# Performance work log

Measured on AMD Instinct MI355X. Metric: run time of the kernel, lower is better.

Reference implementation:

```python
import jax, jax.numpy as jnp
import numpy as np


def setup_inputs() -> dict:
    key = jax.random.key(0)
    k1, k2 = jax.random.split(key)
    decoder_output = jax.random.normal(k1, (8, 2048, 128), dtype=jnp.float32)
    encoder_output = jax.random.normal(k2, (8, 4096, 128), dtype=jnp.float32)
    return {"decoder_output": decoder_output, "encoder_output": encoder_output}


def reference(decoder_output, encoder_output):
    # Unscaled Luong (general dot) attention.
    # scores: [B, Tq, Tk] = dec [B,Tq,D] . enc [B,Tk,D]^T
    scores = jnp.einsum('bqd,bkd->bqk', decoder_output, encoder_output)
    attention = jax.nn.softmax(scores, axis=-1)
    # context: [B, Tq, D] = attn [B,Tq,Tk] . enc [B,Tk,D]
    context = jnp.einsum('bqk,bkd->bqd', attention, encoder_output)
    return (context, attention)
```

## Files before the change

kernel.cpp:

```cpp
#include <hip/hip_runtime.h>

using f16   = _Float16;
using f16x4 = __attribute__((ext_vector_type(4))) _Float16;
using f16x8 = __attribute__((ext_vector_type(8))) _Float16;
using f32x4 = __attribute__((ext_vector_type(4))) float;

#define NBATCH 8
#define TQ 2048
#define TK 4096
#define DD 128
#define QBLK 32
#define KBLK 128
#define NT (TK / KBLK)
#define CTX_ELEMS ((size_t)NBATCH * TQ * DD)
#define PWLD 56
#define CTLD 132

__device__ __forceinline__ int koff(int t, int d) {
    const int blk = ((t >> 2) & 3) ^ ((d >> 4) & 3);
    return (t >> 4) * 2304 + (d >> 4) * 288 + blk * 72 + (t & 3) * 16 + (d & 15);
}

__device__ __forceinline__ f16x4 ds_read_tr16(unsigned addr) {
    f16x4 d;
    asm volatile("ds_read_b64_tr_b16 %0, %1" : "=v"(d) : "v"(addr));
    return d;
}

__global__ __launch_bounds__(256)
void cvt_kernel(const float* __restrict__ in, f16* __restrict__ out) {
    const size_t i = ((size_t)blockIdx.x * 256 + threadIdx.x) * 8;
    const float4 a = *(const float4*)(in + i);
    const float4 b = *(const float4*)(in + i + 4);
    f16x8 h;
    h[0] = (f16)a.x; h[1] = (f16)a.y; h[2] = (f16)a.z; h[3] = (f16)a.w;
    h[4] = (f16)b.x; h[5] = (f16)b.y; h[6] = (f16)b.z; h[7] = (f16)b.w;
    *(f16x8*)(out + i) = h;
}

template<bool F16SRC>
__global__ __launch_bounds__(512, 4)
void luong_attn_kernel(const float* __restrict__ dec,
                       const void* __restrict__ encv,
                       float* __restrict__ out) {
    __shared__ __align__(16) char LDSbuf[36864 + 8 * 16 * PWLD * 2 + 512];
    f16*   Kt    = (f16*)LDSbuf;
    f16*   PwAll = (f16*)(LDSbuf + 36864);
    float* Zbuf  = (float*)(LDSbuf + 36864 + 8 * 16 * PWLD * 2);

    const int tid  = threadIdx.x;
    const int wid  = tid >> 6;
    const int lane = tid & 63;
    const int lo   = lane & 15;
    const int g    = lane >> 4;
    const int qg   = wid & 1;
    const int th   = wid >> 1;

    const int b     = blockIdx.x & 7;
    const int qbase = (blockIdx.x >> 3) * QBLK;

    const float* encB32 = F16SRC ? nullptr : ((const float*)encv) + (size_t)b * TK * DD;
    const f16*   encB16 = F16SRC ? ((const f16*)encv) + (size_t)b * TK * DD : nullptr;
    float* attn = out + CTX_ELEMS + ((size_t)b * TQ + qbase) * TK;

    auto stage = [&](int tile) {
        if constexpr (F16SRC) {
            const f16* src = encB16 + (size_t)tile * KBLK * DD;
            #pragma unroll
            for (int i = 0; i < 4; ++i) {
                const int c = tid + (i << 9);
                const int t = c >> 4;
                const int d0 = (c & 15) << 3;
                *(f16x8*)&Kt[koff(t, d0)] = *(const f16x8*)(src + t * DD + d0);
            }
        } else {
            const float* src = encB32 + (size_t)tile * KBLK * DD;
            #pragma unroll
            for (int i = 0; i < 8; ++i) {
                const int c = tid + (i << 9);
                const int t = c >> 5;
                const int d = (c & 31) << 2;
                const float4 v = *(const float4*)(src + t * DD + d);
                f16x4 h;
                h[0] = (f16)v.x; h[1] = (f16)v.y; h[2] = (f16)v.z; h[3] = (f16)v.w;
                *(f16x4*)&Kt[koff(t, d)] = h;
            }
        }
    };

    const float* qp = dec + ((size_t)b * TQ + qbase + qg * 16 + lo) * DD;
    f16x8 qf[4];
    #pragma unroll
    for (int kk = 0; kk < 4; ++kk) {
        const float4 x = *(const float4*)(qp + kk * 32 + g * 8);
        const float4 y = *(const float4*)(qp + kk * 32 + g * 8 + 4);
        f16x8 h;
        h[0] = (f16)x.x; h[1] = (f16)x.y; h[2] = (f16)x.z; h[3] = (f16)x.w;
        h[4] = (f16)y.x; h[5] = (f16)y.y; h[6] = (f16)y.z; h[7] = (f16)y.w;
        qf[kk] = h;
    }

    float Zp[4] = {0.f, 0.f, 0.f, 0.f};
    #pragma unroll 1
    for (int tile = 0; tile < NT; ++tile) {
        stage(tile);
        __syncthreads();

        f32x4 S[2];
        #pragma unroll
        for (int f = 0; f < 2; ++f) { f32x4 z = {0.f, 0.f, 0.f, 0.f}; S[f] = z; }
        #pragma unroll
        for (int f = 0; f < 2; ++f) {
            const int t = th * 32 + f * 16 + lo;
            #pragma unroll
            for (int kk = 0; kk < 4; ++kk) {
                const f16x8 bf = *(const f16x8*)&Kt[koff(t, kk * 32 + g * 8)];
                S[f] = __builtin_amdgcn_mfma_f32_16x16x32_f16(qf[kk], bf, S[f], 0, 0, 0);
            }
        }
        __syncthreads();

        #pragma unroll
        for (int r = 0; r < 4; ++r)
            Zp[r] += __expf(S[0][r]) + __expf(S[1][r]);
    }

    #pragma unroll
    for (int r = 0; r < 4; ++r) {
        Zp[r] += __shfl_xor(Zp[r], 1);
        Zp[r] += __shfl_xor(Zp[r], 2);
        Zp[r] += __shfl_xor(Zp[r], 4);
        Zp[r] += __shfl_xor(Zp[r], 8);
    }
    if (lo == 0) {
        #pragma unroll
        for (int r = 0; r < 4; ++r) Zbuf[wid * 16 + 4 * g + r] = Zp[r];
    }
    __syncthreads();
    float iz[4];
    #pragma unroll
    for (int r = 0; r < 4; ++r) {
        float z = 0.f;
        #pragma unroll
        for (int t4 = 0; t4 < 4; ++t4) z += Zbuf[(t4 * 2 + qg) * 16 + 4 * g + r];
        iz[r] = 1.0f / z;
    }
    __syncthreads();

    f32x4 ctx[8];
    #pragma unroll
    for (int n = 0; n < 8; ++n) { f32x4 z = {0.f, 0.f, 0.f, 0.f}; ctx[n] = z; }

    f16* Pw = PwAll + wid * 16 * PWLD;
    const unsigned KtBase = (unsigned)(size_t)&Kt[0];
    const int t0 = th * 32 + g * 8;

    #pragma unroll 1
    for (int tile = 0; tile < NT; ++tile) {
        stage(tile);
        __syncthreads();

        f32x4 S[2];
        #pragma unroll
        for (int f = 0; f < 2; ++f) { f32x4 z = {0.f, 0.f, 0.f, 0.f}; S[f] = z; }
        #pragma unroll
        for (int f = 0; f < 2; ++f) {
            const int t = th * 32 + f * 16 + lo;
            #pragma unroll
            for (int kk = 0; kk < 4; ++kk) {
                const f16x8 bf = *(const f16x8*)&Kt[koff(t, kk * 32 + g * 8)];
                S[f] = __builtin_amdgcn_mfma_f32_16x16x32_f16(qf[kk], bf, S[f], 0, 0, 0);
            }
        }

        #pragma unroll
        for (int f = 0; f < 2; ++f) {
            const int tloc = f * 16 + lo;
            #pragma unroll
            for (int r = 0; r < 4; ++r)
                Pw[(4 * g + r) * PWLD + tloc] = (f16)(__expf(S[f][r]) * iz[r]);
        }
        asm volatile("" ::: "memory");

        {
            const int qq  = lane >> 2;
            const int grp = lane & 3;
            const f16x8 pr = *(const f16x8*)&Pw[qq * PWLD + grp * 8];
            f32x4 a0, a1;
            a0[0] = (float)pr[0]; a0[1] = (float)pr[1]; a0[2] = (float)pr[2]; a0[3] = (float)pr[3];
            a1[0] = (float)pr[4]; a1[1] = (float)pr[5]; a1[2] = (float)pr[6]; a1[3] = (float)pr[7];
            float* dst = attn + (size_t)(qg * 16 + qq) * TK + tile * KBLK + th * 32 + grp * 8;
            __builtin_nontemporal_store(a0, (f32x4*)dst);
            __builtin_nontemporal_store(a1, (f32x4*)(dst + 4));
        }

        const f16x8 pa = *(const f16x8*)&Pw[lo * PWLD + g * 8];
        #pragma unroll
        for (int nh = 0; nh < 2; ++nh) {
            f16x4 tr0[4], tr1[4];
            #pragma unroll
            for (int n4 = 0; n4 < 4; ++n4) {
                const int n = nh * 4 + n4;
                const int blk0 = ((t0 >> 2) & 3) ^ (n & 3);
                const int blk1 = (((t0 + 4) >> 2) & 3) ^ (n & 3);
                const unsigned a0 =
                    KtBase + (unsigned)(((t0 >> 4) * 2304 + n * 288 + blk0 * 72) * 2) + lo * 8;
                const unsigned a1 =
                    KtBase + (unsigned)(((t0 >> 4) * 2304 + n * 288 + blk1 * 72) * 2) + lo * 8;
                tr0[n4] = ds_read_tr16(a0);
                tr1[n4] = ds_read_tr16(a1);
            }
            asm volatile("s_waitcnt lgkmcnt(0)" ::: "memory");
            __builtin_amdgcn_sched_barrier(0);
            #pragma unroll
            for (int n4 = 0; n4 < 4; ++n4) {
                f16x8 vb;
                vb[0] = tr0[n4][0]; vb[1] = tr0[n4][1]; vb[2] = tr0[n4][2]; vb[3] = tr0[n4][3];
                vb[4] = tr1[n4][0]; vb[5] = tr1[n4][1]; vb[6] = tr1[n4][2]; vb[7] = tr1[n4][3];
                ctx[nh * 4 + n4] =
                    __builtin_amdgcn_mfma_f32_16x16x32_f16(pa, vb, ctx[nh * 4 + n4], 0, 0, 0);
            }
        }
        __syncthreads();
    }

    float* CT = (float*)LDSbuf;
    const int q32 = qg * 16 + 4 * g;
    if (th >= 2) {
        #pragma unroll
        for (int n = 0; n < 8; ++n)
            #pragma unroll
            for (int r = 0; r < 4; ++r)
                CT[((th - 2) * 32 + q32 + r) * CTLD + n * 16 + lo] = ctx[n][r];
    }
    __syncthreads();
    if (th < 2) {
        #pragma unroll
        for (int n = 0; n < 8; ++n)
            #pragma unroll
            for (int r = 0; r < 4; ++r)
                ctx[n][r] += CT[(th * 32 + q32 + r) * CTLD + n * 16 + lo];
    }
    __syncthreads();
    if (th == 1) {
        #pragma unroll
        for (int n = 0; n < 8; ++n)
            #pragma unroll
            for (int r = 0; r < 4; ++r)
                CT[(q32 + r) * CTLD + n * 16 + lo] = ctx[n][r];
    }
    __syncthreads();
    if (th == 0) {
        #pragma unroll
        for (int n = 0; n < 8; ++n)
            #pragma unroll
            for (int r = 0; r < 4; ++r)
                out[((size_t)b * TQ + qbase + q32 + r) * DD + n * 16 + lo] =
                    ctx[n][r] + CT[(q32 + r) * CTLD + n * 16 + lo];
    }
}

extern "C" void kernel_launch(void* const* d_in, const int* in_sizes, int n_in,
                              void* d_out, int out_size, void* d_ws, size_t ws_size,
                              hipStream_t stream) {
    (void)in_sizes; (void)n_in; (void)out_size;
    const float* dec = (const float*)d_in[0];
    const float* enc = (const float*)d_in[1];
    float* out = (float*)d_out;
    dim3 grid(NBATCH * (TQ / QBLK));
    dim3 block(512);

    const size_t encN = (size_t)NBATCH * TK * DD;
    if (ws_size >= encN * sizeof(f16)) {
        f16* encH = (f16*)d_ws;
        hipLaunchKernelGGL(cvt_kernel, dim3((unsigned)(encN / (256 * 8))), dim3(256),
                           0, stream, enc, encH);
        hipLaunchKernelGGL((luong_attn_kernel<true>), grid, block, 0, stream,
                           dec, (const void*)encH, out);
    } else {
        hipLaunchKernelGGL((luong_attn_kernel<false>), grid, block, 0, stream,
                           dec, (const void*)enc, out);
    }
}
```

Measured before the change: 125.0 us.

## Double-buffer encoder tiles with async global_load_lds prefetch in both passes

Replaces the synchronous per-tile staging of encoder tiles into LDS with a double-buffered pipeline. The f16 path issues direct global-to-LDS loads for the next tile while the current one is computed. The LDS layout drops its padding (2304 to 2048 per row group) so each tile is a contiguous block suited to direct LDS writes, and a barrier per tile is removed. The cost is twice the LDS footprint, which may lower occupancy. Custom vmcnt waits (including vmcnt(2) in the second pass, which seems to wait on the attention stores) add correctness risk, and the unpadded layout may bring back bank conflicts.

```diff
diff --git a/kernel.cpp b/kernel.cpp
--- a/kernel.cpp
+++ b/kernel.cpp
@@ -15,10 +15,12 @@
 #define CTX_ELEMS ((size_t)NBATCH * TQ * DD)
 #define PWLD 56
 #define CTLD 132
+#define KTILE_B 32768
+#define KTILE_E 16384
 
 __device__ __forceinline__ int koff(int t, int d) {
     const int blk = ((t >> 2) & 3) ^ ((d >> 4) & 3);
-    return (t >> 4) * 2304 + (d >> 4) * 288 + blk * 72 + (t & 3) * 16 + (d & 15);
+    return (t >> 4) * 2048 + (d >> 4) * 256 + blk * 64 + (t & 3) * 16 + (d & 15);
 }
 
 __device__ __forceinline__ f16x4 ds_read_tr16(unsigned addr) {
@@ -26,6 +28,13 @@
     asm volatile("ds_read_b64_tr_b16 %0, %1" : "=v"(d) : "v"(addr));
     return d;
 }
+
+__device__ __forceinline__ void pipe_barrier() {
+    asm volatile("s_waitcnt lgkmcnt(0)" ::: "memory");
+    __builtin_amdgcn_s_barrier();
+    __builtin_amdgcn_sched_barrier(0);
+}
+#define VMWAIT(N) asm volatile("s_waitcnt vmcnt(" #N ")" ::: "memory")
 
 __global__ __launch_bounds__(256)
 void cvt_kernel(const float* __restrict__ in, f16* __restrict__ out) {
@@ -43,10 +52,9 @@
 void luong_attn_kernel(const float* __restrict__ dec,
                        const void* __restrict__ encv,
                        float* __restrict__ out) {
-    __shared__ __align__(16) char LDSbuf[36864 + 8 * 16 * PWLD * 2 + 512];
-    f16*   Kt    = (f16*)LDSbuf;
-    f16*   PwAll = (f16*)(LDSbuf + 36864);
-    float* Zbuf  = (float*)(LDSbuf + 36864 + 8 * 16 * PWLD * 2);
+    __shared__ __align__(16) char LDSbuf[2 * KTILE_B + 8 * 16 * PWLD * 2 + 512];
+    f16*   PwAll = (f16*)(LDSbuf + 2 * KTILE_B);
+    float* Zbuf  = (float*)(LDSbuf + 2 * KTILE_B + 8 * 16 * PWLD * 2);
 
     const int tid  = threadIdx.x;
     const int wid  = tid >> 6;
@@ -63,18 +71,29 @@
     const f16*   encB16 = F16SRC ? ((const f16*)encv) + (size_t)b * TK * DD : nullptr;
     float* attn = out + CTX_ELEMS + ((size_t)b * TQ + qbase) * TK;
 
-    auto stage = [&](int tile) {
+    int goff[4];
+    #pragma unroll
+    for (int i = 0; i < 4; ++i) {
+        const int e0 = i * 4096 + tid * 8;
+        const int ts = e0 >> 11, r = e0 & 2047;
+        const int ds = r >> 8,  r2 = r & 255;
+        const int blk = r2 >> 6, row = (r2 >> 4) & 3, colh = (r2 >> 3) & 1;
+        const int t = (ts << 4) + ((blk ^ (ds & 3)) << 2) + row;
+        goff[i] = t * DD + (ds << 4) + colh * 8;
+    }
+
+    auto stage = [&](int cur, int tile) {
         if constexpr (F16SRC) {
-            const f16* src = encB16 + (size_t)tile * KBLK * DD;
-            #pragma unroll
-            for (int i = 0; i < 4; ++i) {
-                const int c = tid + (i << 9);
-                const int t = c >> 4;
-                const int d0 = (c & 15) << 3;
-                *(f16x8*)&Kt[koff(t, d0)] = *(const f16x8*)(src + t * DD + d0);
-            }
+            const f16* src = encB16 + (size_t)tile * KTILE_E;
+            #pragma unroll
+            for (int i = 0; i < 4; ++i)
+                __builtin_amdgcn_global_load_lds(
+                    (const __attribute__((address_space(1))) void*)(src + goff[i]),
+                    (__attribute__((address_space(3))) void*)(LDSbuf + cur * KTILE_B + i * 8192 + wid * 1024),
+                    16, 0, 0);
         } else {
-            const float* src = encB32 + (size_t)tile * KBLK * DD;
+            f16* Kt = (f16*)(LDSbuf + cur * KTILE_B);
+            const float* src = encB32 + (size_t)tile * KTILE_E;
             #pragma unroll
             for (int i = 0; i < 8; ++i) {
                 const int c = tid + (i << 9);
@@ -101,10 +120,14 @@
     }
 
     float Zp[4] = {0.f, 0.f, 0.f, 0.f};
+    stage(0, 0);
+    VMWAIT(0);
+    pipe_barrier();
+    int cur = 0;
     #pragma unroll 1
     for (int tile = 0; tile < NT; ++tile) {
-        stage(tile);
-        __syncthreads();
+        if (tile + 1 < NT) stage(cur ^ 1, tile + 1);
+        const f16* Ktc = (const f16*)(LDSbuf + cur * KTILE_B);
 
         f32x4 S[2];
         #pragma unroll
@@ -114,15 +137,17 @@
             const int t = th * 32 + f * 16 + lo;
             #pragma unroll
             for (int kk = 0; kk < 4; ++kk) {
-                const f16x8 bf = *(const f16x8*)&Kt[koff(t, kk * 32 + g * 8)];
+                const f16x8 bf = *(const f16x8*)&Ktc[koff(t, kk * 32 + g * 8)];
                 S[f] = __builtin_amdgcn_mfma_f32_16x16x32_f16(qf[kk], bf, S[f], 0, 0, 0);
             }
         }
-        __syncthreads();
-
         #pragma unroll
         for (int r = 0; r < 4; ++r)
             Zp[r] += __expf(S[0][r]) + __expf(S[1][r]);
+
+        VMWAIT(0);
+        pipe_barrier();
+        cur ^= 1;
     }
 
     #pragma unroll
@@ -145,20 +170,24 @@
         for (int t4 = 0; t4 < 4; ++t4) z += Zbuf[(t4 * 2 + qg) * 16 + 4 * g + r];
         iz[r] = 1.0f / z;
     }
-    __syncthreads();
 
     f32x4 ctx[8];
     #pragma unroll
     for (int n = 0; n < 8; ++n) { f32x4 z = {0.f, 0.f, 0.f, 0.f}; ctx[n] = z; }
 
     f16* Pw = PwAll + wid * 16 * PWLD;
-    const unsigned KtBase = (unsigned)(size_t)&Kt[0];
+    const unsigned KtLow = (unsigned)(size_t)&LDSbuf[0];
     const int t0 = th * 32 + g * 8;
 
+    stage(0, 0);
+    VMWAIT(0);
+    pipe_barrier();
+    cur = 0;
     #pragma unroll 1
     for (int tile = 0; tile < NT; ++tile) {
-        stage(tile);
-        __syncthreads();
+        if (tile + 1 < NT) stage(cur ^ 1, tile + 1);
+        const f16* Ktc = (const f16*)(LDSbuf + cur * KTILE_B);
+        const unsigned kbase = KtLow + cur * KTILE_B;
 
         f32x4 S[2];
         #pragma unroll
@@ -168,7 +197,7 @@
             const int t = th * 32 + f * 16 + lo;
             #pragma unroll
             for (int kk = 0; kk < 4; ++kk) {
-                const f16x8 bf = *(const f16x8*)&Kt[koff(t, kk * 32 + g * 8)];
+                const f16x8 bf = *(const f16x8*)&Ktc[koff(t, kk * 32 + g * 8)];
                 S[f] = __builtin_amdgcn_mfma_f32_16x16x32_f16(qf[kk], bf, S[f], 0, 0, 0);
             }
         }
@@ -204,9 +233,9 @@
                 const int blk0 = ((t0 >> 2) & 3) ^ (n & 3);
                 const int blk1 = (((t0 + 4) >> 2) & 3) ^ (n & 3);
                 const unsigned a0 =
-                    KtBase + (unsigned)(((t0 >> 4) * 2304 + n * 288 + blk0 * 72) * 2) + lo * 8;
+                    kbase + (unsigned)(((t0 >> 4) * 2048 + n * 256 + blk0 * 64) * 2) + lo * 8;
                 const unsigned a1 =
-                    KtBase + (unsigned)(((t0 >> 4) * 2304 + n * 288 + blk1 * 72) * 2) + lo * 8;
+                    kbase + (unsigned)(((t0 >> 4) * 2048 + n * 256 + blk1 * 64) * 2) + lo * 8;
                 tr0[n4] = ds_read_tr16(a0);
                 tr1[n4] = ds_read_tr16(a1);
             }
@@ -221,7 +250,10 @@
                     __builtin_amdgcn_mfma_f32_16x16x32_f16(pa, vb, ctx[nh * 4 + n4], 0, 0, 0);
             }
         }
-        __syncthreads();
+
+        VMWAIT(2);
+        pipe_barrier();
+        cur ^= 1;
     }
 
     float* CT = (float*)LDSbuf;
```

After: 150.1 us. 1.2x slower.

## Double-buffer encoder tiles in normalizer pass and raise MFMA wave priority

Applied to the files above, without the earlier changes.

In the first (softmax normalizer) pass, the next encoder tile is now loaded into registers while the current tile's score MFMAs run. It is then written into a second LDS buffer, replacing two block barriers per tile with one. The second pass keeps a single buffer but uses the same register-staged load and a leaner barrier. s_setprio is raised around the MFMA sections. The second buffer aliases the P scratch area and grows LDS per block from about 51 KB to about 74 KB, which may cut how many blocks fit on a CU.

```diff
diff --git a/kernel.cpp b/kernel.cpp
--- a/kernel.cpp
+++ b/kernel.cpp
@@ -15,6 +15,7 @@
 #define CTX_ELEMS ((size_t)NBATCH * TQ * DD)
 #define PWLD 56
 #define CTLD 132
+#define KTB 36864
 
 __device__ __forceinline__ int koff(int t, int d) {
     const int blk = ((t >> 2) & 3) ^ ((d >> 4) & 3);
@@ -25,6 +26,12 @@
     f16x4 d;
     asm volatile("ds_read_b64_tr_b16 %0, %1" : "=v"(d) : "v"(addr));
     return d;
+}
+
+__device__ __forceinline__ void pipe_barrier() {
+    asm volatile("s_waitcnt lgkmcnt(0)" ::: "memory");
+    __builtin_amdgcn_s_barrier();
+    __builtin_amdgcn_sched_barrier(0);
 }
 
 __global__ __launch_bounds__(256)
@@ -43,10 +50,11 @@
 void luong_attn_kernel(const float* __restrict__ dec,
                        const void* __restrict__ encv,
                        float* __restrict__ out) {
-    __shared__ __align__(16) char LDSbuf[36864 + 8 * 16 * PWLD * 2 + 512];
-    f16*   Kt    = (f16*)LDSbuf;
-    f16*   PwAll = (f16*)(LDSbuf + 36864);
-    float* Zbuf  = (float*)(LDSbuf + 36864 + 8 * 16 * PWLD * 2);
+    __shared__ __align__(16) char LDSbuf[2 * KTB + 512];
+    f16*   Kt0   = (f16*)LDSbuf;
+    f16*   Kt1   = (f16*)(LDSbuf + KTB);
+    f16*   PwAll = (f16*)(LDSbuf + KTB);
+    float* Zbuf  = (float*)(LDSbuf + 2 * KTB);
 
     const int tid  = threadIdx.x;
     const int wid  = tid >> 6;
@@ -63,27 +71,40 @@
     const f16*   encB16 = F16SRC ? ((const f16*)encv) + (size_t)b * TK * DD : nullptr;
     float* attn = out + CTX_ELEMS + ((size_t)b * TQ + qbase) * TK;
 
-    auto stage = [&](int tile) {
+    f16x8  s16[4];
+    float4 s32[8];
+    auto loadR = [&](int tile) {
         if constexpr (F16SRC) {
             const f16* src = encB16 + (size_t)tile * KBLK * DD;
             #pragma unroll
             for (int i = 0; i < 4; ++i) {
                 const int c = tid + (i << 9);
-                const int t = c >> 4;
-                const int d0 = (c & 15) << 3;
-                *(f16x8*)&Kt[koff(t, d0)] = *(const f16x8*)(src + t * DD + d0);
+                s16[i] = *(const f16x8*)(src + (c >> 4) * DD + ((c & 15) << 3));
             }
         } else {
             const float* src = encB32 + (size_t)tile * KBLK * DD;
             #pragma unroll
             for (int i = 0; i < 8; ++i) {
                 const int c = tid + (i << 9);
-                const int t = c >> 5;
-                const int d = (c & 31) << 2;
-                const float4 v = *(const float4*)(src + t * DD + d);
+                s32[i] = *(const float4*)(src + (c >> 5) * DD + ((c & 31) << 2));
+            }
+        }
+    };
+    auto writeR = [&](f16* Kt) {
+        if constexpr (F16SRC) {
+            #pragma unroll
+            for (int i = 0; i < 4; ++i) {
+                const int c = tid + (i << 9);
+                *(f16x8*)&Kt[koff(c >> 4, (c & 15) << 3)] = s16[i];
+            }
+        } else {
+            #pragma unroll
+            for (int i = 0; i < 8; ++i) {
+                const int c = tid + (i << 9);
                 f16x4 h;
-                h[0] = (f16)v.x; h[1] = (f16)v.y; h[2] = (f16)v.z; h[3] = (f16)v.w;
-                *(f16x4*)&Kt[koff(t, d)] = h;
+                h[0] = (f16)s32[i].x; h[1] = (f16)s32[i].y;
+                h[2] = (f16)s32[i].z; h[3] = (f16)s32[i].w;
+                *(f16x4*)&Kt[koff(c >> 5, (c & 31) << 2)] = h;
             }
         }
     };
@@ -101,28 +122,35 @@
     }
 
     float Zp[4] = {0.f, 0.f, 0.f, 0.f};
+    loadR(0);
+    writeR(Kt0);
+    pipe_barrier();
     #pragma unroll 1
     for (int tile = 0; tile < NT; ++tile) {
-        stage(tile);
-        __syncthreads();
+        f16* Ktc = (tile & 1) ? Kt1 : Kt0;
+        f16* Ktn = (tile & 1) ? Kt0 : Kt1;
+        if (tile + 1 < NT) loadR(tile + 1);
 
         f32x4 S[2];
         #pragma unroll
         for (int f = 0; f < 2; ++f) { f32x4 z = {0.f, 0.f, 0.f, 0.f}; S[f] = z; }
+        __builtin_amdgcn_s_setprio(1);
         #pragma unroll
         for (int f = 0; f < 2; ++f) {
             const int t = th * 32 + f * 16 + lo;
             #pragma unroll
             for (int kk = 0; kk < 4; ++kk) {
-                const f16x8 bf = *(const f16x8*)&Kt[koff(t, kk * 32 + g * 8)];
+                const f16x8 bf = *(const f16x8*)&Ktc[koff(t, kk * 32 + g * 8)];
                 S[f] = __builtin_amdgcn_mfma_f32_16x16x32_f16(qf[kk], bf, S[f], 0, 0, 0);
             }
         }
-        __syncthreads();
-
+        __builtin_amdgcn_s_setprio(0);
+
+        if (tile + 1 < NT) writeR(Ktn);
         #pragma unroll
         for (int r = 0; r < 4; ++r)
             Zp[r] += __expf(S[0][r]) + __expf(S[1][r]);
+        pipe_barrier();
     }
 
     #pragma unroll
@@ -152,26 +180,29 @@
     for (int n = 0; n < 8; ++n) { f32x4 z = {0.f, 0.f, 0.f, 0.f}; ctx[n] = z; }
 
     f16* Pw = PwAll + wid * 16 * PWLD;
-    const unsigned KtBase = (unsigned)(size_t)&Kt[0];
+    const unsigned KtBase = (unsigned)(size_t)&Kt0[0];
     const int t0 = th * 32 + g * 8;
 
     #pragma unroll 1
     for (int tile = 0; tile < NT; ++tile) {
-        stage(tile);
-        __syncthreads();
+        loadR(tile);
+        writeR(Kt0);
+        pipe_barrier();
 
         f32x4 S[2];
         #pragma unroll
         for (int f = 0; f < 2; ++f) { f32x4 z = {0.f, 0.f, 0.f, 0.f}; S[f] = z; }
+        __builtin_amdgcn_s_setprio(1);
         #pragma unroll
         for (int f = 0; f < 2; ++f) {
             const int t = th * 32 + f * 16 + lo;
             #pragma unroll
             for (int kk = 0; kk < 4; ++kk) {
-                const f16x8 bf = *(const f16x8*)&Kt[koff(t, kk * 32 + g * 8)];
+                const f16x8 bf = *(const f16x8*)&Kt0[koff(t, kk * 32 + g * 8)];
                 S[f] = __builtin_amdgcn_mfma_f32_16x16x32_f16(qf[kk], bf, S[f], 0, 0, 0);
             }
         }
+        __builtin_amdgcn_s_setprio(0);
 
         #pragma unroll
         for (int f = 0; f < 2; ++f) {
@@ -195,6 +226,7 @@
         }
 
         const f16x8 pa = *(const f16x8*)&Pw[lo * PWLD + g * 8];
+        __builtin_amdgcn_s_setprio(1);
         #pragma unroll
         for (int nh = 0; nh < 2; ++nh) {
             f16x4 tr0[4], tr1[4];
@@ -221,7 +253,8 @@
                     __builtin_amdgcn_mfma_f32_16x16x32_f16(pa, vb, ctx[nh * 4 + n4], 0, 0, 0);
             }
         }
-        __syncthreads();
+        __builtin_amdgcn_s_setprio(0);
+        pipe_barrier();
     }
 
     float* CT = (float*)LDSbuf;
```

New measurement: 122.7 us. About the same (-1.9%).
